# Kernel tuning notes

Measured on AMD Instinct MI355X. Metric: run time of the kernel, lower is better.

## Reference

```python
import jax, jax.numpy as jnp
import numpy as np

TEMP = 1.0
MEM = 1000           # memory_size
DIM = 128            # embedding_dim
MARGIN = 0.2
NC = 21              # num_classes
HARD_RATIO = 0.8
K_EASY = int(MEM // 5 * (1 - HARD_RATIO))   # 40
K_HARD = int(MEM // 5 * HARD_RATIO)         # 160
A = K_EASY + K_HARD                          # 200 sampled anchors
EPS = 1e-8


def _nearest_down(x, h, w):
    # torch F.interpolate(mode='nearest') downscale: src = floor(dst*H_in/H_out)
    B, H, W = x.shape
    ri = jnp.arange(h) * H // h
    ci = jnp.arange(w) * W // w
    return x[:, ri[:, None], ci[None, :]]


def _pick_first(mask, k):
    # deterministic stand-in for sampling_mask: first k True indices
    n = mask.shape[0]
    score = jnp.where(mask, -jnp.arange(n, dtype=jnp.float32), -jnp.inf)
    _, idx = jax.lax.top_k(score, k)
    return idx, mask[idx]


def setup_inputs() -> dict:
    key = jax.random.key(0)
    ks = jax.random.split(key, 5)
    return {
        "preds": jax.random.normal(ks[0], (8, NC, 512, 512), jnp.float32),
        "embeddings": jax.random.normal(ks[1], (8, DIM, 128, 128), jnp.float32),
        "wsss_gts": jax.random.randint(ks[2], (8, 512, 512), 0, NC, jnp.int32),
        "fsss_gts": jax.random.randint(ks[3], (8, 512, 512), 0, NC, jnp.int32),
        "memory": jax.random.normal(ks[4], (NC - 1, MEM, DIM), jnp.float32),
    }


def reference(preds, embeddings, wsss_gts, fsss_gts, memory):
    B, D, h, w = embeddings.shape
    s_wsss = _nearest_down(wsss_gts, h, w).reshape(-1)                    # [N]
    s_pred = _nearest_down(preds.argmax(axis=1), h, w).reshape(-1)        # [N]
    s_fsss = _nearest_down(fsss_gts, h, w).reshape(-1)                    # [N]

    # L2-normalize embeddings over channel dim, flatten to [N, D]
    emb = embeddings / jnp.maximum(
        jnp.linalg.norm(embeddings, axis=1, keepdims=True), 1e-12)
    emb = emb.transpose(1, 0, 2, 3).reshape(D, -1).T                       # [N, D]

    fg = (s_fsss != 0) & (s_fsss != 255)
    valid_lbl = (s_wsss != 0) & (s_wsss != 255)
    # original loop body overwrites cls with the FIRST (smallest) fg class
    cls = jnp.min(jnp.where(valid_lbl, s_wsss, NC)).astype(jnp.int32)

    anc = (s_wsss == cls) & fg
    easy = anc & (s_pred == cls)
    hard = anc & ~(s_pred == cls)
    ei, ev = _pick_first(easy, K_EASY)
    hi, hv = _pick_first(hard, K_HARD)
    idx = jnp.concatenate([ei, hi])                                        # [A]
    valid = jnp.concatenate([ev, hv])                                      # [A]
    anchors = emb[idx]                                                     # [A, D] (unit norm)

    mem_n = memory / jnp.maximum(
        jnp.linalg.norm(memory, axis=-1, keepdims=True), EPS)
    # all anchor-vs-memory cosine similarities in one batched matmul
    sims = jnp.einsum('ad,cmd->acm', anchors, mem_n)                       # [A, NC-1, MEM]
    pos = sims[:, cls - 1, :]                                              # [A, MEM]
    neg_mask = (jnp.arange(NC - 1) != (cls - 1))
    neg = jnp.where(neg_mask[None, :, None], sims, -jnp.inf).reshape(A, -1)
    hard_neg, _ = jax.lax.top_k(neg, MEM)                                  # [A, MEM] hardest

    # all (pos, hard_neg) pairs per anchor: relu(pos - neg + margin)
    pair = jnp.maximum(pos[:, :, None] - hard_neg[:, None, :] + MARGIN, 0.0)  # [A,MEM,MEM]
    per_anchor = pair.mean(axis=(1, 2))
    vf = valid.astype(pair.dtype)
    loss = jnp.sum(per_anchor * vf) / jnp.maximum(jnp.sum(vf), 1.0)

    # circular memory update for class `cls` (ptr starts at 0); invalid -> dropped
    wpos = jnp.cumsum(valid.astype(jnp.int32)) - 1
    widx = jnp.where(valid, wpos % MEM, MEM)
    new_memory = memory.at[cls - 1, widx].set(
        jax.lax.stop_gradient(anchors), mode='drop')
    return loss, new_memory
```

## Files before the change

kernel.cpp:

```cpp
#include <hip/hip_runtime.h>
#include <stdint.h>

#define NCK 21
#define K_EASY 39
#define K_HARD 160
#define A_TOT  199
#define MARGINF 0.2f

#define OFF_EASY   64
#define OFF_HARD   256
#define OFF_PERA   1024
#define OFF_FLAGS1 4096
#define OFF_FLAGS2 135168
#define OFF_ANCH   266240
#define OFF_SIMS   409600

__device__ __forceinline__ unsigned int f2key(float f) {
  unsigned int u = __float_as_uint(f);
  return u ^ ((u & 0x80000000u) ? 0xFFFFFFFFu : 0x80000000u);
}
__device__ __forceinline__ float key2f(unsigned int k) {
  unsigned int u = (k & 0x80000000u) ? (k ^ 0x80000000u) : (k ^ 0xFFFFFFFFu);
  return __uint_as_float(u);
}

__global__ void k_init(int* hdr) {
  if (threadIdx.x == 0) hdr[0] = NCK;
}

__global__ void k_prep(const int* __restrict__ wsss, const int* __restrict__ fsss,
                       unsigned char* __restrict__ flags1, int* __restrict__ hdr) {
  int p = blockIdx.x * 256 + threadIdx.x;
  int b = p >> 14, r = p & 16383, i = r >> 7, j = r & 127;
  int gi = (b * 512 + i * 4) * 512 + j * 4;
  int w = wsss[gi];
  int f = fsss[gi];
  int fg = (f != 0 && f != 255) ? 1 : 0;
  int wl = (w != 0 && w != 255) ? 1 : 0;
  flags1[p] = (unsigned char)((w & 63) | (fg << 6));
  int cand = wl ? w : NCK;
  for (int off = 32; off > 0; off >>= 1) cand = min(cand, __shfl_down(cand, off));
  __shared__ int wmin[4];
  int lane = threadIdx.x & 63, wid = threadIdx.x >> 6;
  if (lane == 0) wmin[wid] = cand;
  __syncthreads();
  if (threadIdx.x == 0) {
    int m = min(min(wmin[0], wmin[1]), min(wmin[2], wmin[3]));
    atomicMin(&hdr[0], m);
  }
}

__global__ void k_flags(const float* __restrict__ preds, const unsigned char* __restrict__ flags1,
                        unsigned char* __restrict__ flags2, const int* __restrict__ hdr) {
  int p = blockIdx.x * 256 + threadIdx.x;
  int cls = hdr[0];
  unsigned char f1 = flags1[p];
  unsigned char out = 0;
  if ((f1 & 64) && (int)(f1 & 63) == cls) {
    int b = p >> 14, r = p & 16383, i = r >> 7, j = r & 127;
    int base = ((b * NCK) * 512 + i * 4) * 512 + j * 4;
    float best = preds[base]; int bi = 0;
#pragma unroll
    for (int ch = 1; ch < NCK; ++ch) {
      float v = preds[base + ch * 262144];
      if (v > best) { best = v; bi = ch; }
    }
    out = (bi == cls) ? 1 : 2;
  }
  flags2[p] = out;
}

__global__ void k_pick(const unsigned char* __restrict__ flags2, int* __restrict__ hdr,
                       int* __restrict__ easy_idx, int* __restrict__ hard_idx) {
  int lane = threadIdx.x;
  const unsigned long long* f8 = (const unsigned long long*)flags2;
  unsigned int runE = 0, runH = 0;
  for (int it4 = 0; it4 < 64; ++it4) {
    unsigned long long vv0 = f8[(it4 * 4 + 0) * 64 + lane];
    unsigned long long vv1 = f8[(it4 * 4 + 1) * 64 + lane];
    unsigned long long vv2 = f8[(it4 * 4 + 2) * 64 + lane];
    unsigned long long vv3 = f8[(it4 * 4 + 3) * 64 + lane];
#pragma unroll
    for (int q = 0; q < 4; ++q) {
      unsigned long long v = (q == 0) ? vv0 : (q == 1) ? vv1 : (q == 2) ? vv2 : vv3;
      int it = it4 * 4 + q;
      unsigned int e = 0, h = 0;
#pragma unroll
      for (int g = 0; g < 8; ++g) {
        unsigned int b = (unsigned int)((v >> (8 * g)) & 255ull);
        e += (b == 1u); h += (b == 2u);
      }
      unsigned int x = (e << 16) | h;
      unsigned int incl = x;
#pragma unroll
      for (int off = 1; off < 64; off <<= 1) {
        unsigned int t = __shfl_up(incl, off);
        if (lane >= off) incl += t;
      }
      unsigned int excl = incl - x;
      unsigned int eRk = runE + (excl >> 16);
      unsigned int hRk = runH + (excl & 0xFFFFu);
#pragma unroll
      for (int g = 0; g < 8; ++g) {
        unsigned int b = (unsigned int)((v >> (8 * g)) & 255ull);
        int p = it * 512 + lane * 8 + g;
        if (b == 1u)      { if (eRk < K_EASY) easy_idx[eRk] = p; eRk++; }
        else if (b == 2u) { if (hRk < K_HARD) hard_idx[hRk] = p; hRk++; }
      }
      unsigned int tot = __shfl(incl, 63);
      runE += (tot >> 16); runH += (tot & 0xFFFFu);
    }
    if (runE >= K_EASY && runH >= K_HARD) break;
  }
  if (lane == 0) {
    int neU = runE < K_EASY ? (int)runE : K_EASY;
    int nhU = runH < K_HARD ? (int)runH : K_HARD;
    hdr[1] = (int)runE; hdr[2] = (int)runH;
    hdr[3] = neU; hdr[4] = nhU; hdr[5] = neU + nhU;
  }
}

__global__ void k_anchors(const float* __restrict__ emb, const int* __restrict__ hdr,
                          const int* __restrict__ easy_idx, const int* __restrict__ hard_idx,
                          float* __restrict__ anchors) {
  int a = blockIdx.x;
  int tid = threadIdx.x;
  int nv = hdr[5], neU = hdr[3];
  float v0 = 0.f, v1 = 0.f;
  if (a < nv) {
    int p = (a < neU) ? easy_idx[a] : hard_idx[a - neU];
    int b = p >> 14, r = p & 16383, i = r >> 7, j = r & 127;
    int base = b * 2097152 + i * 128 + j;
    v0 = emb[base + tid * 16384];
    v1 = emb[base + (tid + 64) * 16384];
  }
  float ss = v0 * v0 + v1 * v1;
  for (int off = 32; off > 0; off >>= 1) ss += __shfl_xor(ss, off);
  float inv = 1.0f / fmaxf(sqrtf(ss), 1e-12f);
  anchors[a * 128 + tid] = v0 * inv;
  anchors[a * 128 + tid + 64] = v1 * inv;
}

__global__ __launch_bounds__(256) void k_sims(const float* __restrict__ anchors,
                       const float* __restrict__ memory, float* __restrict__ sims,
                       int a0, int ac) {
  __shared__ float As[64 * 128];
  __shared__ float Ms[64 * 128];
  int mT = blockIdx.x, aT = blockIdx.y;
  int aBase = aT * 64, mBase = mT * 64;
  int tid = threadIdx.x;
#pragma unroll
  for (int k = 0; k < 8; ++k) {
    int f4i = tid + k * 256;
    int row = f4i >> 5, c = f4i & 31;
    int gR = a0 + aBase + row; if (gR > 255) gR = 255;
    float4 v = ((const float4*)anchors)[gR * 32 + c];
    *(float4*)&As[row * 128 + ((c ^ (row & 31)) << 2)] = v;
  }
#pragma unroll
  for (int k = 0; k < 8; ++k) {
    int f4i = tid + k * 256;
    int row = f4i >> 5, c = f4i & 31;
    int grow = mBase + row;
    float4 v = make_float4(0.f, 0.f, 0.f, 0.f);
    if (grow < 20000) v = ((const float4*)memory)[grow * 32 + c];
    *(float4*)&Ms[row * 128 + ((c ^ (row & 31)) << 2)] = v;
  }
  __syncthreads();
  int tx = tid & 15, ty = tid >> 4;
  float acc[4][4];
#pragma unroll
  for (int i = 0; i < 4; ++i)
#pragma unroll
    for (int j = 0; j < 4; ++j) acc[i][j] = 0.f;
#pragma unroll 2
  for (int c = 0; c < 32; ++c) {
    float4 av[4], mv[4];
#pragma unroll
    for (int i = 0; i < 4; ++i) {
      int ar = ty + 16 * i;
      av[i] = *(const float4*)&As[ar * 128 + ((c ^ (ar & 31)) << 2)];
    }
#pragma unroll
    for (int j = 0; j < 4; ++j) {
      int mr = tx + 16 * j;
      mv[j] = *(const float4*)&Ms[mr * 128 + ((c ^ (mr & 31)) << 2)];
    }
#pragma unroll
    for (int i = 0; i < 4; ++i)
#pragma unroll
      for (int j = 0; j < 4; ++j)
        acc[i][j] += av[i].x * mv[j].x + av[i].y * mv[j].y + av[i].z * mv[j].z + av[i].w * mv[j].w;
  }
  __syncthreads();
  {
    int row = tid >> 2, q = tid & 3;
    float ss = 0.f;
#pragma unroll
    for (int k = 0; k < 8; ++k) {
      float4 v = *(const float4*)&Ms[row * 128 + q * 32 + k * 4];
      ss += v.x * v.x + v.y * v.y + v.z * v.z + v.w * v.w;
    }
    ss += __shfl_down(ss, 2, 4);
    ss += __shfl_down(ss, 1, 4);
    if (q == 0) As[row] = 1.0f / fmaxf(sqrtf(ss), 1e-8f);
  }
  __syncthreads();
#pragma unroll
  for (int i = 0; i < 4; ++i) {
    int la = aBase + ty + 16 * i;
    if (la < ac) {
#pragma unroll
      for (int j = 0; j < 4; ++j) {
        int m = mBase + tx + 16 * j;
        if (m < 20000) sims[(size_t)la * 20000 + m] = acc[i][j] * As[tx + 16 * j];
      }
    }
  }
}

__device__ __forceinline__ void suffix_select(unsigned int* histL, unsigned int* sfx,
                                              unsigned int* cnts, int tid, unsigned int krem) {
  if (tid < 64) {
    int lane = tid;
    unsigned int h0 = histL[lane * 4 + 0];
    unsigned int h1 = histL[lane * 4 + 1];
    unsigned int h2 = histL[lane * 4 + 2];
    unsigned int h3 = histL[lane * 4 + 3];
    unsigned int s = h0 + h1 + h2 + h3;
    unsigned int incl = s;
#pragma unroll
    for (int off = 1; off < 64; off <<= 1) {
      unsigned int t = __shfl_down(incl, off);
      if (lane + off < 64) incl += t;
    }
    unsigned int above = incl - s;
    unsigned int f3 = above + h3;
    unsigned int f2 = f3 + h2;
    unsigned int f1 = f2 + h1;
    unsigned int f0 = f1 + h0;
    sfx[lane * 4 + 0] = f0; sfx[lane * 4 + 1] = f1;
    sfx[lane * 4 + 2] = f2; sfx[lane * 4 + 3] = f3;
    if (lane == 63) sfx[256] = 0u;
    if (f0 >= krem && f1 < krem)    cnts[3] = (unsigned int)(lane * 4 + 0);
    if (f1 >= krem && f2 < krem)    cnts[3] = (unsigned int)(lane * 4 + 1);
    if (f2 >= krem && f3 < krem)    cnts[3] = (unsigned int)(lane * 4 + 2);
    if (f3 >= krem && above < krem) cnts[3] = (unsigned int)(lane * 4 + 3);
  }
  __syncthreads();
}

__global__ __launch_bounds__(1024) void k_topk(const float* __restrict__ sims,
                       const int* __restrict__ hdr, float* __restrict__ per_anchor,
                       int a0, int ac) {
  int la = blockIdx.x;
  if (la >= ac) return;
  int a = a0 + la;
  int nv = hdr[5];
  if (a >= nv) return;
  int clsRow = hdr[0] - 1;
  int tid = threadIdx.x, lane = tid & 63, wid = tid >> 6;

  __shared__ float posArr[1024];
  __shared__ float qv[1024];
  __shared__ unsigned int hist16[16][256];
  __shared__ unsigned int histL[256];
  __shared__ unsigned int sfx[257];
  __shared__ unsigned int buf[12288];
  __shared__ unsigned int cnts[8];
  __shared__ float fred[16];

  const float* row = sims + (size_t)la * 20000;

  for (int i = tid; i < 16 * 256; i += 1024) ((unsigned int*)hist16)[i] = 0u;
  if (tid < 24) posArr[1000 + tid] = -1e30f;
  if (tid < 8) cnts[tid] = 0u;
  __syncthreads();

  float4 rowq[5];
#pragma unroll
  for (int k = 0; k < 5; ++k) {
    int j = (k << 12) + (tid << 2);
    float4 v = make_float4(0.f, 0.f, 0.f, 0.f);
    if (j < 20000) v = *(const float4*)&row[j];
    rowq[k] = v;
  }
#pragma unroll
  for (int k = 0; k < 5; ++k) {
    int j = (k << 12) + (tid << 2);
    if (j < 20000) {
      int c = j / 1000;
      float4 v = rowq[k];
      if (c == clsRow) {
        *(float4*)&posArr[j - clsRow * 1000] = v;
      } else {
        atomicAdd(&hist16[wid][f2key(v.x) >> 24], 1u);
        atomicAdd(&hist16[wid][f2key(v.y) >> 24], 1u);
        atomicAdd(&hist16[wid][f2key(v.z) >> 24], 1u);
        atomicAdd(&hist16[wid][f2key(v.w) >> 24], 1u);
      }
    }
  }
  __syncthreads();
  if (tid < 256) {
    unsigned int s = 0;
#pragma unroll
    for (int w = 0; w < 16; ++w) s += hist16[w][tid];
    histL[tid] = s;
  }
  __syncthreads();
  suffix_select(histL, sfx, cnts, tid, 1000u);
  unsigned int B0 = cnts[3];
  unsigned int krem = 1000u - sfx[B0 + 1];
  __syncthreads();

#pragma unroll
  for (int k = 0; k < 5; ++k) {
    int j = (k << 12) + (tid << 2);
    bool inb = (j < 20000);
    int c = inb ? (j / 1000) : -1;
    bool neg = inb && (c != clsRow);
    float4 v4 = rowq[k];
#pragma unroll
    for (int e = 0; e < 4; ++e) {
      float v = (e == 0) ? v4.x : (e == 1) ? v4.y : (e == 2) ? v4.z : v4.w;
      unsigned int key = f2key(v);
      unsigned int tb = key >> 24;
      bool pq = neg && (tb > B0);
      bool pb = neg && (tb == B0);
      unsigned long long mq = __ballot(pq);
      unsigned long long mb = __ballot(pb);
      unsigned int baseq = 0u, baseb = 0u;
      if (lane == 0) {
        if (mq) baseq = atomicAdd(&cnts[2], (unsigned int)__popcll(mq));
        if (mb) baseb = atomicAdd(&cnts[1], (unsigned int)__popcll(mb));
      }
      baseq = __shfl(baseq, 0); baseb = __shfl(baseb, 0);
      if (pq) qv[baseq + (unsigned int)__popcll(mq & ((1ull << lane) - 1ull))] = v;
      if (pb) {
        unsigned int p = baseb + (unsigned int)__popcll(mb & ((1ull << lane) - 1ull));
        if (p < 12288u) buf[p] = key;
      }
    }
  }
  __syncthreads();
  int ncand = (int)cnts[1];
  bool stored = (ncand <= 12288);

  unsigned int prefix = B0 << 24;
  for (int level = 0; level < 3; ++level) {
    int shift = 16 - level * 8;
    if (tid < 256) histL[tid] = 0u;
    __syncthreads();
    unsigned int myk[12];
    if (stored) {
#pragma unroll
      for (int k = 0; k < 12; ++k) {
        int i = tid + (k << 10);
        if (i < ncand) myk[k] = buf[i];
      }
      __syncthreads();
#pragma unroll
      for (int k = 0; k < 12; ++k) {
        int i = tid + (k << 10);
        if (i < ncand) atomicAdd(&histL[(myk[k] >> shift) & 255u], 1u);
      }
    } else {
      unsigned int hiMask = 0xFFFFFFFFu << (shift + 8);
      for (int j = tid; j < 20000; j += 1024) {
        int c = j / 1000;
        if (c == clsRow) continue;
        unsigned int key = f2key(row[j]);
        if ((key & hiMask) == prefix) atomicAdd(&histL[(key >> shift) & 255u], 1u);
      }
    }
    __syncthreads();
    suffix_select(histL, sfx, cnts, tid, krem);
    unsigned int bk = cnts[3];
    unsigned int above = sfx[bk + 1];
    krem -= above;
    prefix |= bk << shift;
    if (stored) {
      __syncthreads();
      if (tid == 0) cnts[4] = 0u;
      __syncthreads();
#pragma unroll
      for (int k = 0; k < 12; ++k) {
        int i = tid + (k << 10);
        if (i < ncand) {
          unsigned int b = (myk[k] >> shift) & 255u;
          if (b > bk) qv[atomicAdd(&cnts[2], 1u)] = key2f(myk[k]);
          else if (b == bk) buf[atomicAdd(&cnts[4], 1u)] = myk[k];
        }
      }
      __syncthreads();
      ncand = (int)cnts[4];
    }
  }
  float tval = key2f(prefix);

  if (!stored) {
    for (int j = tid; j < 20000; j += 1024) {
      int c = j / 1000;
      if (c == clsRow) continue;
      float v = row[j];
      unsigned int key = f2key(v);
      if ((key >> 24) == B0 && key > prefix) qv[atomicAdd(&cnts[2], 1u) & 1023u] = v;
    }
    __syncthreads();
  }
  int qn = (int)cnts[2];
  float tieW = (float)krem;

  float v, w;
  if (tid < qn)       { v = qv[tid]; w = 1.f; }
  else if (tid == qn) { v = tval;    w = tieW; }
  else                { v = 0.f;     w = 0.f; }
  float t = v - MARGINF;
  float s0 = 0.f, s1 = 0.f, s2 = 0.f, s3 = 0.f;
  if (w != 0.f) {
    for (int pc = 0; pc < 1024; pc += 16) {
      float4 p0 = *(const float4*)&posArr[pc];
      float4 p1 = *(const float4*)&posArr[pc + 4];
      float4 p2 = *(const float4*)&posArr[pc + 8];
      float4 p3 = *(const float4*)&posArr[pc + 12];
      s0 += fmaxf(p0.x - t, 0.f); s1 += fmaxf(p0.y - t, 0.f);
      s2 += fmaxf(p0.z - t, 0.f); s3 += fmaxf(p0.w - t, 0.f);
      s0 += fmaxf(p1.x - t, 0.f); s1 += fmaxf(p1.y - t, 0.f);
      s2 += fmaxf(p1.z - t, 0.f); s3 += fmaxf(p1.w - t, 0.f);
      s0 += fmaxf(p2.x - t, 0.f); s1 += fmaxf(p2.y - t, 0.f);
      s2 += fmaxf(p2.z - t, 0.f); s3 += fmaxf(p2.w - t, 0.f);
      s0 += fmaxf(p3.x - t, 0.f); s1 += fmaxf(p3.y - t, 0.f);
      s2 += fmaxf(p3.z - t, 0.f); s3 += fmaxf(p3.w - t, 0.f);
    }
  }
  float local = w * ((s0 + s1) + (s2 + s3));
  for (int off = 32; off; off >>= 1) local += __shfl_down(local, off);
  if (lane == 0) fred[wid] = local;
  __syncthreads();
  if (tid == 0) {
    float s = 0.f;
#pragma unroll
    for (int i = 0; i < 16; ++i) s += fred[i];
    per_anchor[a] = s * 1e-6f;
  }
}

__global__ void k_loss(const float* __restrict__ per_anchor, const int* __restrict__ hdr,
                       float* __restrict__ out) {
  int nv = hdr[5];
  int tid = threadIdx.x;
  float s = (tid < nv) ? per_anchor[tid] : 0.f;
  for (int off = 32; off; off >>= 1) s += __shfl_down(s, off);
  __shared__ float fr[4];
  if ((tid & 63) == 0) fr[tid >> 6] = s;
  __syncthreads();
  if (tid == 0) out[0] = (fr[0] + fr[1] + fr[2] + fr[3]) / (float)max(nv, 1);
}

__global__ void k_writemem(const float* __restrict__ memory, const float* __restrict__ anchors,
                           const int* __restrict__ hdr, float* __restrict__ out) {
  int cls = hdr[0], nv = hdr[5];
  int i = blockIdx.x * 1024 + threadIdx.x;
#pragma unroll
  for (int k = 0; k < 4; ++k, i += 256) {
    float v = memory[i];
    int c = i / 128000;
    int rem = i - c * 128000;
    int m = rem >> 7, d = rem & 127;
    if (cls >= 1 && cls <= 20 && c == cls - 1 && m < nv) v = anchors[m * 128 + d];
    out[1 + i] = v;
  }
}

extern "C" void kernel_launch(void* const* d_in, const int* in_sizes, int n_in,
                              void* d_out, int out_size, void* d_ws, size_t ws_size,
                              hipStream_t stream) {
  const float* preds  = (const float*)d_in[0];
  const float* emb    = (const float*)d_in[1];
  const int*   wsss   = (const int*)d_in[2];
  const int*   fsss   = (const int*)d_in[3];
  const float* memory = (const float*)d_in[4];
  float* out = (float*)d_out;
  char* ws = (char*)d_ws;
  int* hdr = (int*)ws;
  int* easy_idx = (int*)(ws + OFF_EASY);
  int* hard_idx = (int*)(ws + OFF_HARD);
  float* per_anchor = (float*)(ws + OFF_PERA);
  unsigned char* flags1 = (unsigned char*)(ws + OFF_FLAGS1);
  unsigned char* flags2 = (unsigned char*)(ws + OFF_FLAGS2);
  float* anchors = (float*)(ws + OFF_ANCH);
  float* sims = (float*)(ws + OFF_SIMS);

  hipLaunchKernelGGL(k_init,    dim3(1),   dim3(64),  0, stream, hdr);
  hipLaunchKernelGGL(k_prep,    dim3(512), dim3(256), 0, stream, wsss, fsss, flags1, hdr);
  hipLaunchKernelGGL(k_flags,   dim3(512), dim3(256), 0, stream, preds, flags1, flags2, hdr);
  hipLaunchKernelGGL(k_pick,    dim3(1),   dim3(64),  0, stream, flags2, hdr, easy_idx, hard_idx);
  hipLaunchKernelGGL(k_anchors, dim3(256), dim3(64),  0, stream, emb, hdr, easy_idx, hard_idx, anchors);

  float* outScr = out + 4;
  int capOut = (int)(((long long)out_size / 4 - 4) / 20000LL);
  if (capOut > 127) capOut = 127;
  if (capOut < 0) capOut = 0;
  long long avail = (long long)ws_size - (long long)OFF_SIMS;
  int capWs = (avail > 0) ? (int)(avail / 80000LL) : 0;
  if (capWs > A_TOT) capWs = A_TOT;
  if (capOut + capWs < 1) capWs = 1;

  int aoff = 0;
  while (aoff < A_TOT) {
    int nOut = A_TOT - aoff; if (nOut > capOut) nOut = capOut;
    int nWs  = A_TOT - aoff - nOut; if (nWs > capWs) nWs = capWs;
    if (nOut > 0) {
      dim3 gs(313, (nOut + 63) / 64);
      hipLaunchKernelGGL(k_sims, gs, dim3(256), 0, stream, anchors, memory, outScr, aoff, nOut);
    }
    if (nWs > 0) {
      dim3 gs(313, (nWs + 63) / 64);
      hipLaunchKernelGGL(k_sims, gs, dim3(256), 0, stream, anchors, memory, sims, aoff + nOut, nWs);
    }
    if (nOut > 0)
      hipLaunchKernelGGL(k_topk, dim3(nOut), dim3(1024), 0, stream, outScr, hdr, per_anchor, aoff, nOut);
    if (nWs > 0)
      hipLaunchKernelGGL(k_topk, dim3(nWs), dim3(1024), 0, stream, sims, hdr, per_anchor, aoff + nOut, nWs);
    aoff += nOut + nWs;
  }

  hipLaunchKernelGGL(k_loss,    dim3(1),    dim3(256), 0, stream, per_anchor, hdr, out);
  hipLaunchKernelGGL(k_writemem,dim3(2500), dim3(256), 0, stream, memory, anchors, hdr, out);
}
```

Before: 422.7 us.

## Fuse init, loss reduction and memory write into neighbouring kernels

Removes the init kernel by having k_prep write per-block minima and k_flags reduce them redundantly per block. The loss reduction moves into k_topk via an atomic last-block counter. When the workspace can hold all anchor rows, the memory copy also moves into k_topk, which cuts launches. The cost is redundant reduction work in every k_flags block and a large copy loop added to the topk blocks, which may lengthen that critical kernel.

```diff
diff --git a/kernel.cpp b/kernel.cpp
--- a/kernel.cpp
+++ b/kernel.cpp
@@ -10,6 +10,7 @@
 #define OFF_EASY   64
 #define OFF_HARD   256
 #define OFF_PERA   1024
+#define OFF_MINARR 2048
 #define OFF_FLAGS1 4096
 #define OFF_FLAGS2 135168
 #define OFF_ANCH   266240
@@ -24,12 +25,8 @@
   return __uint_as_float(u);
 }
 
-__global__ void k_init(int* hdr) {
-  if (threadIdx.x == 0) hdr[0] = NCK;
-}
-
 __global__ void k_prep(const int* __restrict__ wsss, const int* __restrict__ fsss,
-                       unsigned char* __restrict__ flags1, int* __restrict__ hdr) {
+                       unsigned char* __restrict__ flags1, int* __restrict__ minArr) {
   int p = blockIdx.x * 256 + threadIdx.x;
   int b = p >> 14, r = p & 16383, i = r >> 7, j = r & 127;
   int gi = (b * 512 + i * 4) * 512 + j * 4;
@@ -44,16 +41,29 @@
   int lane = threadIdx.x & 63, wid = threadIdx.x >> 6;
   if (lane == 0) wmin[wid] = cand;
   __syncthreads();
-  if (threadIdx.x == 0) {
-    int m = min(min(wmin[0], wmin[1]), min(wmin[2], wmin[3]));
-    atomicMin(&hdr[0], m);
-  }
+  if (threadIdx.x == 0)
+    minArr[blockIdx.x] = min(min(wmin[0], wmin[1]), min(wmin[2], wmin[3]));
 }
 
 __global__ void k_flags(const float* __restrict__ preds, const unsigned char* __restrict__ flags1,
-                        unsigned char* __restrict__ flags2, const int* __restrict__ hdr) {
-  int p = blockIdx.x * 256 + threadIdx.x;
-  int cls = hdr[0];
+                        unsigned char* __restrict__ flags2, const int* __restrict__ minArr,
+                        int* __restrict__ hdr) {
+  int tid = threadIdx.x;
+  __shared__ int wm[4];
+  __shared__ int s_cls;
+  int m = min(minArr[tid], minArr[tid + 256]);
+  for (int off = 32; off > 0; off >>= 1) m = min(m, __shfl_down(m, off));
+  int lane = tid & 63, wid = tid >> 6;
+  if (lane == 0) wm[wid] = m;
+  __syncthreads();
+  if (tid == 0) {
+    int c = min(min(wm[0], wm[1]), min(wm[2], wm[3]));
+    s_cls = c;
+    if (blockIdx.x == 0) { hdr[0] = c; hdr[6] = 0; }
+  }
+  __syncthreads();
+  int cls = s_cls;
+  int p = blockIdx.x * 256 + tid;
   unsigned char f1 = flags1[p];
   unsigned char out = 0;
   if ((f1 & 64) && (int)(f1 & 63) == cls) {
@@ -251,15 +261,32 @@
 }
 
 __global__ __launch_bounds__(1024) void k_topk(const float* __restrict__ sims,
-                       const int* __restrict__ hdr, float* __restrict__ per_anchor,
-                       int a0, int ac) {
+                       int* __restrict__ hdr, float* __restrict__ per_anchor,
+                       int a0, int ac, float* __restrict__ out,
+                       const float* __restrict__ memory, const float* __restrict__ anchors,
+                       int doCopy) {
+  int tid = threadIdx.x, lane = tid & 63, wid = tid >> 6;
+  int nv = hdr[5];
+  int cls = hdr[0];
+
+  if (doCopy) {
+    int step = gridDim.x * 1024;
+    for (int i = blockIdx.x * 1024 + tid; i < 2560000; i += step) {
+      float v = memory[i];
+      int c = i / 128000;
+      int rem = i - c * 128000;
+      int m = rem >> 7, d = rem & 127;
+      if (cls >= 1 && cls <= 20 && c == cls - 1 && m < nv) v = anchors[m * 128 + d];
+      out[1 + i] = v;
+    }
+    if (nv == 0 && blockIdx.x == 0 && tid == 0) out[0] = 0.f;
+  }
+
   int la = blockIdx.x;
   if (la >= ac) return;
   int a = a0 + la;
-  int nv = hdr[5];
   if (a >= nv) return;
-  int clsRow = hdr[0] - 1;
-  int tid = threadIdx.x, lane = tid & 63, wid = tid >> 6;
+  int clsRow = cls - 1;
 
   __shared__ float posArr[1024];
   __shared__ float qv[1024];
@@ -269,6 +296,7 @@
   __shared__ unsigned int buf[12288];
   __shared__ unsigned int cnts[8];
   __shared__ float fred[16];
+  __shared__ unsigned int lastFlag;
 
   const float* row = sims + (size_t)la * 20000;
 
@@ -443,24 +471,30 @@
 #pragma unroll
     for (int i = 0; i < 16; ++i) s += fred[i];
     per_anchor[a] = s * 1e-6f;
-  }
-}
-
-__global__ void k_loss(const float* __restrict__ per_anchor, const int* __restrict__ hdr,
-                       float* __restrict__ out) {
-  int nv = hdr[5];
-  int tid = threadIdx.x;
-  float s = (tid < nv) ? per_anchor[tid] : 0.f;
-  for (int off = 32; off; off >>= 1) s += __shfl_down(s, off);
-  __shared__ float fr[4];
-  if ((tid & 63) == 0) fr[tid >> 6] = s;
-  __syncthreads();
-  if (tid == 0) out[0] = (fr[0] + fr[1] + fr[2] + fr[3]) / (float)max(nv, 1);
+    __threadfence();
+    unsigned int tk = atomicAdd((unsigned int*)&hdr[6], 1u);
+    lastFlag = (tk == (unsigned int)(nv - 1)) ? 1u : 0u;
+  }
+  __syncthreads();
+  if (lastFlag) {
+    __threadfence();
+    float s = (tid < nv) ? per_anchor[tid] : 0.f;
+    for (int off = 32; off; off >>= 1) s += __shfl_down(s, off);
+    if (lane == 0) fred[wid] = s;
+    __syncthreads();
+    if (tid == 0) {
+      float tot = 0.f;
+#pragma unroll
+      for (int i = 0; i < 16; ++i) tot += fred[i];
+      out[0] = tot / (float)max(nv, 1);
+    }
+  }
 }
 
 __global__ void k_writemem(const float* __restrict__ memory, const float* __restrict__ anchors,
                            const int* __restrict__ hdr, float* __restrict__ out) {
   int cls = hdr[0], nv = hdr[5];
+  if (nv == 0 && blockIdx.x == 0 && threadIdx.x == 0) out[0] = 0.f;
   int i = blockIdx.x * 1024 + threadIdx.x;
 #pragma unroll
   for (int k = 0; k < 4; ++k, i += 256) {
@@ -487,45 +521,52 @@
   int* easy_idx = (int*)(ws + OFF_EASY);
   int* hard_idx = (int*)(ws + OFF_HARD);
   float* per_anchor = (float*)(ws + OFF_PERA);
+  int* minArr = (int*)(ws + OFF_MINARR);
   unsigned char* flags1 = (unsigned char*)(ws + OFF_FLAGS1);
   unsigned char* flags2 = (unsigned char*)(ws + OFF_FLAGS2);
   float* anchors = (float*)(ws + OFF_ANCH);
   float* sims = (float*)(ws + OFF_SIMS);
 
-  hipLaunchKernelGGL(k_init,    dim3(1),   dim3(64),  0, stream, hdr);
-  hipLaunchKernelGGL(k_prep,    dim3(512), dim3(256), 0, stream, wsss, fsss, flags1, hdr);
-  hipLaunchKernelGGL(k_flags,   dim3(512), dim3(256), 0, stream, preds, flags1, flags2, hdr);
+  hipLaunchKernelGGL(k_prep,    dim3(512), dim3(256), 0, stream, wsss, fsss, flags1, minArr);
+  hipLaunchKernelGGL(k_flags,   dim3(512), dim3(256), 0, stream, preds, flags1, flags2, minArr, hdr);
   hipLaunchKernelGGL(k_pick,    dim3(1),   dim3(64),  0, stream, flags2, hdr, easy_idx, hard_idx);
   hipLaunchKernelGGL(k_anchors, dim3(256), dim3(64),  0, stream, emb, hdr, easy_idx, hard_idx, anchors);
 
-  float* outScr = out + 4;
-  int capOut = (int)(((long long)out_size / 4 - 4) / 20000LL);
-  if (capOut > 127) capOut = 127;
-  if (capOut < 0) capOut = 0;
   long long avail = (long long)ws_size - (long long)OFF_SIMS;
   int capWs = (avail > 0) ? (int)(avail / 80000LL) : 0;
   if (capWs > A_TOT) capWs = A_TOT;
-  if (capOut + capWs < 1) capWs = 1;
-
-  int aoff = 0;
-  while (aoff < A_TOT) {
-    int nOut = A_TOT - aoff; if (nOut > capOut) nOut = capOut;
-    int nWs  = A_TOT - aoff - nOut; if (nWs > capWs) nWs = capWs;
-    if (nOut > 0) {
-      dim3 gs(313, (nOut + 63) / 64);
-      hipLaunchKernelGGL(k_sims, gs, dim3(256), 0, stream, anchors, memory, outScr, aoff, nOut);
-    }
-    if (nWs > 0) {
-      dim3 gs(313, (nWs + 63) / 64);
-      hipLaunchKernelGGL(k_sims, gs, dim3(256), 0, stream, anchors, memory, sims, aoff + nOut, nWs);
-    }
-    if (nOut > 0)
-      hipLaunchKernelGGL(k_topk, dim3(nOut), dim3(1024), 0, stream, outScr, hdr, per_anchor, aoff, nOut);
-    if (nWs > 0)
-      hipLaunchKernelGGL(k_topk, dim3(nWs), dim3(1024), 0, stream, sims, hdr, per_anchor, aoff + nOut, nWs);
-    aoff += nOut + nWs;
-  }
-
-  hipLaunchKernelGGL(k_loss,    dim3(1),    dim3(256), 0, stream, per_anchor, hdr, out);
-  hipLaunchKernelGGL(k_writemem,dim3(2500), dim3(256), 0, stream, memory, anchors, hdr, out);
-}
+
+  if (capWs >= A_TOT) {
+    dim3 gs(313, (A_TOT + 63) / 64);
+    hipLaunchKernelGGL(k_sims, gs, dim3(256), 0, stream, anchors, memory, sims, 0, A_TOT);
+    hipLaunchKernelGGL(k_topk, dim3(A_TOT), dim3(1024), 0, stream, sims, hdr, per_anchor,
+                       0, A_TOT, out, memory, anchors, 1);
+  } else {
+    float* outScr = out + 4;
+    int capOut = (int)(((long long)out_size / 4 - 4) / 20000LL);
+    if (capOut > 127) capOut = 127;
+    if (capOut < 0) capOut = 0;
+    if (capOut + capWs < 1) capWs = 1;
+    int aoff = 0;
+    while (aoff < A_TOT) {
+      int nOut = A_TOT - aoff; if (nOut > capOut) nOut = capOut;
+      int nWs  = A_TOT - aoff - nOut; if (nWs > capWs) nWs = capWs;
+      if (nOut > 0) {
+        dim3 g1(313, (nOut + 63) / 64);
+        hipLaunchKernelGGL(k_sims, g1, dim3(256), 0, stream, anchors, memory, outScr, aoff, nOut);
+      }
+      if (nWs > 0) {
+        dim3 g2(313, (nWs + 63) / 64);
+        hipLaunchKernelGGL(k_sims, g2, dim3(256), 0, stream, anchors, memory, sims, aoff + nOut, nWs);
+      }
+      if (nOut > 0)
+        hipLaunchKernelGGL(k_topk, dim3(nOut), dim3(1024), 0, stream, outScr, hdr, per_anchor,
+                           aoff, nOut, out, memory, anchors, 0);
+      if (nWs > 0)
+        hipLaunchKernelGGL(k_topk, dim3(nWs), dim3(1024), 0, stream, sims, hdr, per_anchor,
+                           aoff + nOut, nWs, out, memory, anchors, 0);
+      aoff += nOut + nWs;
+    }
+    hipLaunchKernelGGL(k_writemem, dim3(2500), dim3(256), 0, stream, memory, anchors, hdr, out);
+  }
+}
```

New measurement: 373.3 us, median of 2. 1.13x faster.
